# Kernel optimization log

Measured on AMD Instinct MI355X. Metric: run time of the kernel, lower is better.

The kernel has to match this reference:

```python
import jax, jax.numpy as jnp
import numpy as np

D_IN = 2048
D_OUT = 2048
LN_EPS = 1e-5


def setup_inputs() -> dict:
    key = jax.random.key(0)
    kx, kw, kb = jax.random.split(key, 3)
    x = jax.random.normal(kx, (8, 2048, D_IN), dtype=jnp.float32)
    # LayerNorm affine params (torch defaults: ones / zeros)
    gamma = jnp.ones((D_IN,), dtype=jnp.float32)
    beta = jnp.zeros((D_IN,), dtype=jnp.float32)
    # weight = rand(out,in)*0.001, bias = rand(out)*0.001, alpha = ones(out)
    weight = jax.random.uniform(kw, (D_OUT, D_IN), dtype=jnp.float32) * 0.001
    bias = jax.random.uniform(kb, (D_OUT,), dtype=jnp.float32) * 0.001
    alpha = jnp.ones((D_OUT,), dtype=jnp.float32)
    return {"x": x, "gamma": gamma, "beta": beta, "weight": weight,
            "bias": bias, "alpha": alpha}


def reference(x, gamma, beta, weight, bias, alpha):
    # LayerNorm over last dim (biased variance, eps=1e-5, affine)
    mu = jnp.mean(x, axis=-1, keepdims=True)
    var = jnp.mean(jnp.square(x - mu), axis=-1, keepdims=True)
    xn = (x - mu) * jax.lax.rsqrt(var + LN_EPS) * gamma + beta
    # Binarize activations: hard sign
    a = jnp.sign(xn)
    # Binarize weights: mean-center per output row, clip, sign (STE in fwd == sign)
    centered = weight - jnp.mean(weight, axis=1, keepdims=True)  # [O, I]
    signed_w = jnp.sign(centered)
    # Linear + bias, then per-output-channel alpha scale
    out = jnp.einsum('bsi,oi->bso', a, signed_w) + bias
    return out * alpha
```

## Files before the change

### kernel.cpp

```cpp
#include <hip/hip_runtime.h>

#define DIN 2048
#define WPR 64
#define QPR 32
#define GPR 16
#define RPB 8
#define LN_EPS 1e-5f

#define GLOBAL_AS __attribute__((address_space(1)))
#define LDS_AS    __attribute__((address_space(3)))

typedef unsigned long long u64;
typedef int   i32x4  __attribute__((ext_vector_type(4)));
typedef int   i32x8  __attribute__((ext_vector_type(8)));
typedef float f32x16 __attribute__((ext_vector_type(16)));

__device__ inline float wave_sum(float v) {
    #pragma unroll
    for (int off = 32; off; off >>= 1) v += __shfl_down(v, off, 64);
    return v;
}


__global__ __launch_bounds__(256) void expand_kernel(const float* __restrict__ x,
                                                     const float* __restrict__ gamma,
                                                     const float* __restrict__ beta,
                                                     const float* __restrict__ w,
                                                     char* __restrict__ Aexp,
                                                     char* __restrict__ Bexp,
                                                     int Mblocks) {
    const int t = threadIdx.x;
    const int wid = t >> 6, lane = t & 63;
    __shared__ float red[4][2 * RPB];
    __shared__ __align__(16) unsigned stg[RPB * 256];

    const bool isA = (int)blockIdx.x < Mblocks;
    const int r0 = (isA ? (int)blockIdx.x : ((int)blockIdx.x - Mblocks)) * RPB;
    const float* src = isA ? x : w;

    float gg[8], bb[8];
    if (isA) {
        float4 g0 = ((const float4*)gamma)[t * 2];
        float4 g1 = ((const float4*)gamma)[t * 2 + 1];
        float4 b0 = ((const float4*)beta)[t * 2];
        float4 b1 = ((const float4*)beta)[t * 2 + 1];
        gg[0]=g0.x; gg[1]=g0.y; gg[2]=g0.z; gg[3]=g0.w;
        gg[4]=g1.x; gg[5]=g1.y; gg[6]=g1.z; gg[7]=g1.w;
        bb[0]=b0.x; bb[1]=b0.y; bb[2]=b0.z; bb[3]=b0.w;
        bb[4]=b1.x; bb[5]=b1.y; bb[6]=b1.z; bb[7]=b1.w;
    }

    float vv[RPB][8];
    #pragma unroll
    for (int rr = 0; rr < RPB; ++rr) {
        const float* xr = src + (size_t)(r0 + rr) * DIN;
        float4 v0 = ((const float4*)xr)[t * 2];
        float4 v1 = ((const float4*)xr)[t * 2 + 1];
        vv[rr][0]=v0.x; vv[rr][1]=v0.y; vv[rr][2]=v0.z; vv[rr][3]=v0.w;
        vv[rr][4]=v1.x; vv[rr][5]=v1.y; vv[rr][6]=v1.z; vv[rr][7]=v1.w;
    }

    #pragma unroll
    for (int rr = 0; rr < RPB; ++rr) {
        float s = 0.f, ss = 0.f;
        #pragma unroll
        for (int j = 0; j < 8; ++j) s += vv[rr][j];
        if (isA) {
            #pragma unroll
            for (int j = 0; j < 8; ++j) ss += vv[rr][j] * vv[rr][j];
        }
        s = wave_sum(s);
        if (isA) ss = wave_sum(ss);
        if (lane == 0) { red[wid][rr * 2] = s; red[wid][rr * 2 + 1] = ss; }
    }
    __syncthreads();

    #pragma unroll
    for (int rr = 0; rr < RPB; ++rr) {
        float tot = red[0][rr*2] + red[1][rr*2] + red[2][rr*2] + red[3][rr*2];
        float mu  = tot * (1.f / DIN);
        unsigned word = 0;
        if (isA) {
            float tots = red[0][rr*2+1] + red[1][rr*2+1] + red[2][rr*2+1] + red[3][rr*2+1];
            float var  = tots * (1.f / DIN) - mu * mu;
            float rs   = rsqrtf(var + LN_EPS);
            #pragma unroll
            for (int j = 0; j < 8; ++j) {
                float xn = (vv[rr][j] - mu) * rs * gg[j] + bb[j];
                word |= (xn < 0.f ? 0xAu : 0x2u) << (4 * j);
            }
        } else {
            #pragma unroll
            for (int j = 0; j < 8; ++j)
                word |= ((vv[rr][j] - mu) < 0.f ? 0xAu : 0x2u) << (4 * j);
        }
        stg[rr * 256 + (((t >> 2) ^ rr) << 2) + (t & 3)] = word;
    }
    __syncthreads();

    char* dstbase = isA ? Aexp : Bexp;
    const int bm  = r0 >> 8;
    const int rt  = (r0 >> 5) & 7;
    const int ri0 = r0 & 31;
    #pragma unroll
    for (int i2 = 0; i2 < 2; ++i2) {
        const int u  = i2 * 256 + t;
        const int sc = u >> 5;
        const int kt = (u >> 4) & 1, hb = (u >> 3) & 1, ri = u & 7;
        const int g  = sc * 4 + kt * 2 + hb;
        uint4 v = *(const uint4*)&stg[ri * 256 + ((g ^ ri) << 2)];
        const size_t doff = (((size_t)(bm * 16 + sc)) * 8 + rt) * 2048 + kt * 1024 +
                            (ri0 + ri + 32 * hb) * 16;
        *(uint4*)(dstbase + doff) = v;
    }
}

__global__ __launch_bounds__(256, 3) void fp4gemm_kernel(const char* __restrict__ Aexp,
                                                         const char* __restrict__ Bexp,
                                                         const float* __restrict__ bias,
                                                         const float* __restrict__ alpha,
                                                         float* __restrict__ out,
                                                         int ldc, int nBmX) {
    __shared__ char As[3][8192];
    __shared__ char Bs[3][8192];
    const int t = threadIdx.x;
    const int wv = t >> 6, lane = t & 63;
    const int xcd = blockIdx.x & 7;
    const int loc = blockIdx.x >> 3;
    const int bm = xcd * nBmX + (loc % nBmX);
    const int bn = loc / nBmX;
    const int wr = wv >> 1, wc = wv & 1;

    const char* gA = Aexp + (size_t)(bm >> 1) * 262144 + (size_t)(bm & 1) * 8192;
    const char* gB = Bexp + (size_t)(bn >> 1) * 262144 + (size_t)(bn & 1) * 8192;

#define STAGE(BUF, S)                                                           \
    {                                                                           \
        _Pragma("unroll")                                                       \
        for (int i2 = 0; i2 < 2; ++i2) {                                        \
            const int ch = wv * 2 + i2;                                         \
            __builtin_amdgcn_global_load_lds(                                   \
                (const GLOBAL_AS unsigned*)(gA + (size_t)(S) * 16384 + ch * 1024 + lane * 16), \
                (LDS_AS unsigned*)(&As[BUF][ch * 1024]), 16, 0, 0);             \
            __builtin_amdgcn_global_load_lds(                                   \
                (const GLOBAL_AS unsigned*)(gB + (size_t)(S) * 16384 + ch * 1024 + lane * 16), \
                (LDS_AS unsigned*)(&Bs[BUF][ch * 1024]), 16, 0, 0);             \
        }                                                                       \
    }

    f32x16 acc[2][2];
    #pragma unroll
    for (int i = 0; i < 2; ++i)
        #pragma unroll
        for (int j = 0; j < 2; ++j)
            #pragma unroll
            for (int e = 0; e < 16; ++e) acc[i][j][e] = 0.f;

    STAGE(0, 0)
    STAGE(1, 1)
    asm volatile("s_waitcnt vmcnt(4)" ::: "memory");
    __builtin_amdgcn_s_barrier();
    asm volatile("" ::: "memory");

    int c = 0;
    #pragma unroll 1
    for (int s = 0; s < 16; ++s) {
        if (s <= 13) {
            const int nb = (c == 0) ? 2 : c - 1;
            STAGE(nb, s + 2)
        }
        #pragma unroll
        for (int kt = 0; kt < 2; ++kt) {
            i32x4 a[2], b[2];
            #pragma unroll
            for (int i = 0; i < 2; ++i)
                a[i] = *(const i32x4*)&As[c][(wr * 2 + i) * 2048 + kt * 1024 + lane * 16];
            #pragma unroll
            for (int j = 0; j < 2; ++j)
                b[j] = *(const i32x4*)&Bs[c][(wc * 2 + j) * 2048 + kt * 1024 + lane * 16];
            i32x8 aa[2], bb2[2];
            #pragma unroll
            for (int i = 0; i < 2; ++i) {
                aa[i][0]=a[i][0]; aa[i][1]=a[i][1]; aa[i][2]=a[i][2]; aa[i][3]=a[i][3];
                aa[i][4]=a[i][0]; aa[i][5]=a[i][1]; aa[i][6]=a[i][2]; aa[i][7]=a[i][3];
                bb2[i][0]=b[i][0]; bb2[i][1]=b[i][1]; bb2[i][2]=b[i][2]; bb2[i][3]=b[i][3];
                bb2[i][4]=b[i][0]; bb2[i][5]=b[i][1]; bb2[i][6]=b[i][2]; bb2[i][7]=b[i][3];
            }
            __builtin_amdgcn_s_setprio(1);
            #pragma unroll
            for (int i = 0; i < 2; ++i)
                #pragma unroll
                for (int j = 0; j < 2; ++j)
                    acc[i][j] = __builtin_amdgcn_mfma_scale_f32_32x32x64_f8f6f4(
                        aa[i], bb2[j], acc[i][j], 4, 4,
                        0, 0x7F7F7F7F, 0, 0x7F7F7F7F);
            __builtin_amdgcn_s_setprio(0);
        }
        if (s == 15) break;
        if (s <= 13) { asm volatile("s_waitcnt vmcnt(4)" ::: "memory"); }
        else         { asm volatile("s_waitcnt vmcnt(0)" ::: "memory"); }
        __builtin_amdgcn_s_barrier();
        asm volatile("" ::: "memory");
        c = (c == 2) ? 0 : c + 1;
    }
#undef STAGE

    const int cl = lane & 31;
    const int rb = 4 * (lane >> 5);
    #pragma unroll
    for (int i = 0; i < 2; ++i) {
        #pragma unroll
        for (int j = 0; j < 2; ++j) {
            const int col = bn * 128 + wc * 64 + j * 32 + cl;
            const float bi = bias[col], al = alpha[col];
            const int row0 = bm * 128 + wr * 64 + i * 32 + rb;
            #pragma unroll
            for (int reg = 0; reg < 16; ++reg) {
                const int row = row0 + (reg & 3) + 8 * (reg >> 2);
                __builtin_nontemporal_store((acc[i][j][reg] + bi) * al,
                                            &out[(size_t)row * ldc + col]);
            }
        }
    }
}

__global__ __launch_bounds__(256) void w_pack_kernel(const float* __restrict__ w,
                                                     unsigned* __restrict__ wpk) {
    const int row = blockIdx.x;
    const int t = threadIdx.x;
    const float* wr = w + (size_t)row * DIN;
    float4 v0 = ((const float4*)wr)[t * 2];
    float4 v1 = ((const float4*)wr)[t * 2 + 1];
    float s = v0.x + v0.y + v0.z + v0.w + v1.x + v1.y + v1.z + v1.w;

    __shared__ float red[4];
    float wsum = wave_sum(s);
    int wid = t >> 6, lane = t & 63;
    if (lane == 0) red[wid] = wsum;
    __syncthreads();
    float mu = (red[0] + red[1] + red[2] + red[3]) * (1.f / DIN);

    float vv[8] = {v0.x, v0.y, v0.z, v0.w, v1.x, v1.y, v1.z, v1.w};
    unsigned byte = 0;
    #pragma unroll
    for (int j = 0; j < 8; ++j)
        byte |= ((vv[j] - mu) < 0.f ? 1u : 0u) << j;

    __shared__ unsigned char bytes[256];
    bytes[t] = (unsigned char)byte;
    __syncthreads();
    if (t < 64) {
        unsigned wd = (unsigned)bytes[t * 4] | ((unsigned)bytes[t * 4 + 1] << 8) |
                      ((unsigned)bytes[t * 4 + 2] << 16) | ((unsigned)bytes[t * 4 + 3] << 24);
        wpk[(size_t)row * WPR + t] = wd;
    }
}

__global__ __launch_bounds__(256) void ln_pack_kernel(const float* __restrict__ x,
                                                      const float* __restrict__ gamma,
                                                      const float* __restrict__ beta,
                                                      unsigned* __restrict__ apk) {
    const int row = blockIdx.x;
    const int t = threadIdx.x;
    const float* xr = x + (size_t)row * DIN;
    float4 v0 = ((const float4*)xr)[t * 2];
    float4 v1 = ((const float4*)xr)[t * 2 + 1];
    float s  = v0.x + v0.y + v0.z + v0.w + v1.x + v1.y + v1.z + v1.w;
    float ss = v0.x * v0.x + v0.y * v0.y + v0.z * v0.z + v0.w * v0.w +
               v1.x * v1.x + v1.y * v1.y + v1.z * v1.z + v1.w * v1.w;

    __shared__ float red[8];
    float wsum = wave_sum(s), wssum = wave_sum(ss);
    int wid = t >> 6, lane = t & 63;
    if (lane == 0) { red[wid] = wsum; red[4 + wid] = wssum; }
    __syncthreads();
    float tot  = red[0] + red[1] + red[2] + red[3];
    float tots = red[4] + red[5] + red[6] + red[7];
    float mu  = tot * (1.f / DIN);
    float var = tots * (1.f / DIN) - mu * mu;
    float rs  = rsqrtf(var + LN_EPS);

    float4 g0 = ((const float4*)gamma)[t * 2];
    float4 g1 = ((const float4*)gamma)[t * 2 + 1];
    float4 b0 = ((const float4*)beta)[t * 2];
    float4 b1 = ((const float4*)beta)[t * 2 + 1];
    float vv[8] = {v0.x, v0.y, v0.z, v0.w, v1.x, v1.y, v1.z, v1.w};
    float gg[8] = {g0.x, g0.y, g0.z, g0.w, g1.x, g1.y, g1.z, g1.w};
    float bb[8] = {b0.x, b0.y, b0.z, b0.w, b1.x, b1.y, b1.z, b1.w};
    unsigned byte = 0;
    #pragma unroll
    for (int j = 0; j < 8; ++j) {
        float xn = (vv[j] - mu) * rs * gg[j] + bb[j];
        byte |= (xn < 0.f ? 1u : 0u) << j;
    }

    __shared__ unsigned char bytes[256];
    bytes[t] = (unsigned char)byte;
    __syncthreads();
    if (t < 64) {
        unsigned wd = (unsigned)bytes[t * 4] | ((unsigned)bytes[t * 4 + 1] << 8) |
                      ((unsigned)bytes[t * 4 + 2] << 16) | ((unsigned)bytes[t * 4 + 3] << 24);
        apk[(size_t)row * WPR + t] = wd;
    }
}

__global__ __launch_bounds__(256) void bingemm_kernel(const u64* __restrict__ A,
                                                      const u64* __restrict__ B,
                                                      const float* __restrict__ bias,
                                                      const float* __restrict__ alpha,
                                                      float* __restrict__ out) {
    __shared__ u64 S[2 * 128 * QPR];
    uint4* Sg = (uint4*)S;
    const int t = threadIdx.x;
    const int bn = blockIdx.x, bm = blockIdx.y;

    const uint4* Ag = (const uint4*)(A + (size_t)bm * 128 * QPR);
    #pragma unroll
    for (int i = 0; i < 8; ++i) {
        int id = t + i * 256;
        int row = id >> 4, g = id & 15;
        Sg[(row << 4) + (g ^ (row & 15))] = Ag[id];
    }
    const uint4* Bg = (const uint4*)(B + (size_t)bn * 128 * QPR);
    #pragma unroll
    for (int i = 0; i < 8; ++i) {
        int id = t + i * 256;
        int row = id >> 4, g = id & 15;
        Sg[2048 + (row << 4) + (g ^ (row & 15))] = Bg[id];
    }
    __syncthreads();

    const int tr = t >> 4;
    const int tc = t & 15;
    const ulonglong2* Sq = (const ulonglong2*)S;
    const int abase = tr * GPR;
    const int bbase = 2048 + tc * GPR;

    int acc[8][8] = {};
    u64 a0[8][2], b0[8][2], a1[8][2], b1[8][2];

#define LOADK(KK, AR, BR)                                            \
    {                                                                \
        const int ka = abase + ((KK) ^ tr);                          \
        const int kb = bbase + ((KK) ^ tc);                          \
        _Pragma("unroll")                                            \
        for (int r = 0; r < 8; ++r) {                                \
            ulonglong2 v = Sq[ka + r * 256];                         \
            AR[r][0] = v.x; AR[r][1] = v.y;                          \
        }                                                            \
        _Pragma("unroll")                                            \
        for (int c2 = 0; c2 < 8; ++c2) {                             \
            ulonglong2 v = Sq[kb + c2 * 256];                        \
            BR[c2][0] = v.x; BR[c2][1] = v.y;                        \
        }                                                            \
    }

#define COMPK(AR, BR)                                                \
    {                                                                \
        _Pragma("unroll")                                            \
        for (int r = 0; r < 8; ++r) {                                \
            _Pragma("unroll")                                        \
            for (int c2 = 0; c2 < 8; ++c2) {                         \
                acc[r][c2] += __popcll(AR[r][0] ^ BR[c2][0]);        \
                acc[r][c2] += __popcll(AR[r][1] ^ BR[c2][1]);        \
            }                                                        \
        }                                                            \
    }

    LOADK(0, a0, b0);
    #pragma unroll 1
    for (int kk = 0; kk < 14; kk += 2) {
        LOADK(kk + 1, a1, b1);
        COMPK(a0, b0);
        LOADK(kk + 2, a0, b0);
        COMPK(a1, b1);
    }
    LOADK(15, a1, b1);
    COMPK(a0, b0);
    COMPK(a1, b1);
#undef LOADK
#undef COMPK

    float bi[8], al[8];
    #pragma unroll
    for (int c2 = 0; c2 < 8; ++c2) {
        int col = bn * 128 + tc + 16 * c2;
        bi[c2] = bias[col];
        al[c2] = alpha[col];
    }
    #pragma unroll
    for (int r = 0; r < 8; ++r) {
        const size_t row = (size_t)bm * 128 + tr + 16 * r;
        float* op = out + row * 2048 + bn * 128 + tc;
        #pragma unroll
        for (int c2 = 0; c2 < 8; ++c2)
            op[16 * c2] = ((float)(DIN - 2 * acc[r][c2]) + bi[c2]) * al[c2];
    }
}

extern "C" void kernel_launch(void* const* d_in, const int* in_sizes, int n_in,
                              void* d_out, int out_size, void* d_ws, size_t ws_size,
                              hipStream_t stream) {
    const float* x     = (const float*)d_in[0];
    const float* gamma = (const float*)d_in[1];
    const float* beta  = (const float*)d_in[2];
    const float* w     = (const float*)d_in[3];
    const float* bias  = (const float*)d_in[4];
    const float* alpha = (const float*)d_in[5];
    float* out = (float*)d_out;

    const int M = in_sizes[0] / DIN;
    const int N = in_sizes[3] / DIN;

    const size_t needA = (size_t)M * (DIN / 2);
    const size_t needB = (size_t)N * (DIN / 2);

    if (ws_size >= needA + needB && (M % 1024) == 0 && N == 2048) {
        char* Aexp = (char*)d_ws;
        char* Bexp = (char*)d_ws + needA;
        expand_kernel<<<(M + N) / RPB, 256, 0, stream>>>(x, gamma, beta, w,
                                                         Aexp, Bexp, M / RPB);
        const int nBmX = (M / 128) / 8;
        dim3 grid((M / 128) * (N / 128));
        fp4gemm_kernel<<<grid, 256, 0, stream>>>(Aexp, Bexp, bias, alpha, out,
                                                 N, nBmX);
    } else {
        unsigned* apk = (unsigned*)d_ws;
        unsigned* wpk = (unsigned*)((char*)d_ws + (size_t)M * WPR * 4);
        w_pack_kernel<<<N, 256, 0, stream>>>(w, wpk);
        ln_pack_kernel<<<M, 256, 0, stream>>>(x, gamma, beta, apk);
        dim3 grid(N / 128, M / 128);
        bingemm_kernel<<<grid, 256, 0, stream>>>((const u64*)apk, (const u64*)wpk,
                                                 bias, alpha, out);
    }
}
```

Baseline: 83.35 us.

## Load GEMM fragments directly from global into registers, dropping LDS staging

Replaces the three-stage LDS pipeline (global_load_lds plus barriers) with direct per-wave global loads of pre-swizzled fragments into registers, double-buffered in registers across K steps. This removes the LDS round trip, the ds_reads and the workgroup barriers. In exchange, waves that share A or B tiles each fetch the data separately from global/L2, so global traffic rises, and the extra register buffers may reduce occupancy.

```diff
diff --git a/kernel.cpp b/kernel.cpp
--- a/kernel.cpp
+++ b/kernel.cpp
@@ -121,8 +121,6 @@
                                                          const float* __restrict__ alpha,
                                                          float* __restrict__ out,
                                                          int ldc, int nBmX) {
-    __shared__ char As[3][8192];
-    __shared__ char Bs[3][8192];
     const int t = threadIdx.x;
     const int wv = t >> 6, lane = t & 63;
     const int xcd = blockIdx.x & 7;
@@ -131,20 +129,49 @@
     const int bn = loc / nBmX;
     const int wr = wv >> 1, wc = wv & 1;
 
-    const char* gA = Aexp + (size_t)(bm >> 1) * 262144 + (size_t)(bm & 1) * 8192;
-    const char* gB = Bexp + (size_t)(bn >> 1) * 262144 + (size_t)(bn & 1) * 8192;
-
-#define STAGE(BUF, S)                                                           \
+    const char* gA = Aexp + (size_t)(bm >> 1) * 262144 + (size_t)(bm & 1) * 8192 + lane * 16;
+    const char* gB = Bexp + (size_t)(bn >> 1) * 262144 + (size_t)(bn & 1) * 8192 + lane * 16;
+
+#define LOADF(S, AF, BF)                                                        \
     {                                                                           \
         _Pragma("unroll")                                                       \
-        for (int i2 = 0; i2 < 2; ++i2) {                                        \
-            const int ch = wv * 2 + i2;                                         \
-            __builtin_amdgcn_global_load_lds(                                   \
-                (const GLOBAL_AS unsigned*)(gA + (size_t)(S) * 16384 + ch * 1024 + lane * 16), \
-                (LDS_AS unsigned*)(&As[BUF][ch * 1024]), 16, 0, 0);             \
-            __builtin_amdgcn_global_load_lds(                                   \
-                (const GLOBAL_AS unsigned*)(gB + (size_t)(S) * 16384 + ch * 1024 + lane * 16), \
-                (LDS_AS unsigned*)(&Bs[BUF][ch * 1024]), 16, 0, 0);             \
+        for (int kt = 0; kt < 2; ++kt) {                                        \
+            _Pragma("unroll")                                                   \
+            for (int i = 0; i < 2; ++i)                                         \
+                AF[kt][i] = *(const i32x4*)(gA + (size_t)(S) * 16384 +          \
+                                            (wr * 2 + i) * 2048 + kt * 1024);   \
+            _Pragma("unroll")                                                   \
+            for (int j = 0; j < 2; ++j)                                         \
+                BF[kt][j] = *(const i32x4*)(gB + (size_t)(S) * 16384 +          \
+                                            (wc * 2 + j) * 2048 + kt * 1024);   \
+        }                                                                       \
+    }
+
+#define COMPF(AF, BF)                                                           \
+    {                                                                           \
+        _Pragma("unroll")                                                       \
+        for (int kt = 0; kt < 2; ++kt) {                                        \
+            i32x8 aa[2], bb2[2];                                                \
+            _Pragma("unroll")                                                   \
+            for (int i = 0; i < 2; ++i) {                                       \
+                aa[i][0]=AF[kt][i][0]; aa[i][1]=AF[kt][i][1];                   \
+                aa[i][2]=AF[kt][i][2]; aa[i][3]=AF[kt][i][3];                   \
+                aa[i][4]=AF[kt][i][0]; aa[i][5]=AF[kt][i][1];                   \
+                aa[i][6]=AF[kt][i][2]; aa[i][7]=AF[kt][i][3];                   \
+                bb2[i][0]=BF[kt][i][0]; bb2[i][1]=BF[kt][i][1];                 \
+                bb2[i][2]=BF[kt][i][2]; bb2[i][3]=BF[kt][i][3];                 \
+                bb2[i][4]=BF[kt][i][0]; bb2[i][5]=BF[kt][i][1];                 \
+                bb2[i][6]=BF[kt][i][2]; bb2[i][7]=BF[kt][i][3];                 \
+            }                                                                   \
+            __builtin_amdgcn_s_setprio(1);                                      \
+            _Pragma("unroll")                                                   \
+            for (int i = 0; i < 2; ++i)                                         \
+                _Pragma("unroll")                                               \
+                for (int j = 0; j < 2; ++j)                                     \
+                    acc[i][j] = __builtin_amdgcn_mfma_scale_f32_32x32x64_f8f6f4(\
+                        aa[i], bb2[j], acc[i][j], 4, 4,                         \
+                        0, 0x7F7F7F7F, 0, 0x7F7F7F7F);                          \
+            __builtin_amdgcn_s_setprio(0);                                      \
         }                                                                       \
     }
 
@@ -156,54 +183,21 @@
             #pragma unroll
             for (int e = 0; e < 16; ++e) acc[i][j][e] = 0.f;
 
-    STAGE(0, 0)
-    STAGE(1, 1)
-    asm volatile("s_waitcnt vmcnt(4)" ::: "memory");
-    __builtin_amdgcn_s_barrier();
-    asm volatile("" ::: "memory");
-
-    int c = 0;
+    i32x4 af0[2][2], bf0[2][2], af1[2][2], bf1[2][2];
+
+    LOADF(0, af0, bf0)
     #pragma unroll 1
-    for (int s = 0; s < 16; ++s) {
-        if (s <= 13) {
-            const int nb = (c == 0) ? 2 : c - 1;
-            STAGE(nb, s + 2)
-        }
-        #pragma unroll
-        for (int kt = 0; kt < 2; ++kt) {
-            i32x4 a[2], b[2];
-            #pragma unroll
-            for (int i = 0; i < 2; ++i)
-                a[i] = *(const i32x4*)&As[c][(wr * 2 + i) * 2048 + kt * 1024 + lane * 16];
-            #pragma unroll
-            for (int j = 0; j < 2; ++j)
-                b[j] = *(const i32x4*)&Bs[c][(wc * 2 + j) * 2048 + kt * 1024 + lane * 16];
-            i32x8 aa[2], bb2[2];
-            #pragma unroll
-            for (int i = 0; i < 2; ++i) {
-                aa[i][0]=a[i][0]; aa[i][1]=a[i][1]; aa[i][2]=a[i][2]; aa[i][3]=a[i][3];
-                aa[i][4]=a[i][0]; aa[i][5]=a[i][1]; aa[i][6]=a[i][2]; aa[i][7]=a[i][3];
-                bb2[i][0]=b[i][0]; bb2[i][1]=b[i][1]; bb2[i][2]=b[i][2]; bb2[i][3]=b[i][3];
-                bb2[i][4]=b[i][0]; bb2[i][5]=b[i][1]; bb2[i][6]=b[i][2]; bb2[i][7]=b[i][3];
-            }
-            __builtin_amdgcn_s_setprio(1);
-            #pragma unroll
-            for (int i = 0; i < 2; ++i)
-                #pragma unroll
-                for (int j = 0; j < 2; ++j)
-                    acc[i][j] = __builtin_amdgcn_mfma_scale_f32_32x32x64_f8f6f4(
-                        aa[i], bb2[j], acc[i][j], 4, 4,
-                        0, 0x7F7F7F7F, 0, 0x7F7F7F7F);
-            __builtin_amdgcn_s_setprio(0);
-        }
-        if (s == 15) break;
-        if (s <= 13) { asm volatile("s_waitcnt vmcnt(4)" ::: "memory"); }
-        else         { asm volatile("s_waitcnt vmcnt(0)" ::: "memory"); }
-        __builtin_amdgcn_s_barrier();
-        asm volatile("" ::: "memory");
-        c = (c == 2) ? 0 : c + 1;
-    }
-#undef STAGE
+    for (int s = 0; s < 14; s += 2) {
+        LOADF(s + 1, af1, bf1)
+        COMPF(af0, bf0)
+        LOADF(s + 2, af0, bf0)
+        COMPF(af1, bf1)
+    }
+    LOADF(15, af1, bf1)
+    COMPF(af0, bf0)
+    COMPF(af1, bf1)
+#undef LOADF
+#undef COMPF
 
     const int cl = lane & 31;
     const int rb = 4 * (lane >> 5);
```

New measurement: 86.06 us. +3.2%, slower.
